# Kernel optimization log

Hardware: AMD Instinct MI355X
Metric: run time of the kernel (lower is better)

Reference implementation:

```python
import jax, jax.numpy as jnp
import numpy as np

NUM_GROUPS = 32
EPS = 1e-6


def group_norm(x, gamma, beta):
    # x: [b, c, h, w]
    b, c, h, w = x.shape
    xg = x.reshape(b, NUM_GROUPS, c // NUM_GROUPS, h, w)
    mean = jnp.mean(xg, axis=(2, 3, 4), keepdims=True)
    var = jnp.var(xg, axis=(2, 3, 4), keepdims=True)
    xn = ((xg - mean) * jax.lax.rsqrt(var + EPS)).reshape(b, c, h, w)
    return xn * gamma[None, :, None, None] + beta[None, :, None, None]


def setup_inputs() -> dict:
    key = jax.random.key(0)
    ks = jax.random.split(key, 8)
    B, C, H, W = 4, 512, 64, 64
    s = 0.02  # small init so softmax is well-conditioned
    return {
        "x": jax.random.normal(ks[0], (B, C, H, W), dtype=jnp.float32),
        "gamma": jnp.ones((C,), dtype=jnp.float32),
        "beta": jnp.zeros((C,), dtype=jnp.float32),
        "wq": jax.random.normal(ks[1], (C, C), dtype=jnp.float32) * s,
        "bq": jnp.zeros((C,), dtype=jnp.float32),
        "wk": jax.random.normal(ks[2], (C, C), dtype=jnp.float32) * s,
        "bk": jnp.zeros((C,), dtype=jnp.float32),
        "wv": jax.random.normal(ks[3], (C, C), dtype=jnp.float32) * s,
        "bv": jnp.zeros((C,), dtype=jnp.float32),
        "wp": jax.random.normal(ks[4], (C, C), dtype=jnp.float32) * s,
        "bp": jnp.zeros((C,), dtype=jnp.float32),
    }


def reference(x, gamma, beta, wq, bq, wk, bk, wv, bv, wp, bp):
    b, c, h, w = x.shape
    hw = h * w
    h_ = group_norm(x, gamma, beta).reshape(b, c, hw)  # [b, c, hw]
    # 1x1 convs == channel matmuls
    q = jnp.einsum('oc,bcn->bon', wq, h_) + bq[None, :, None]
    k = jnp.einsum('oc,bcn->bon', wk, h_) + bk[None, :, None]
    v = jnp.einsum('oc,bcn->bon', wv, h_) + bv[None, :, None]
    # scores[b, n, m] = sum_c q[b,c,n] k[b,c,m]
    scores = jnp.einsum('bcn,bcm->bnm', q, k) * (c ** -0.5)
    attn = jax.nn.softmax(scores, axis=2)  # over keys m
    # out[b, c, n] = sum_m v[b,c,m] * attn[b,n,m]
    o = jnp.einsum('bcm,bnm->bcn', v, attn)
    o = jnp.einsum('oc,bcn->bon', wp, o) + bp[None, :, None]
    return x + o.reshape(b, c, h, w)
```

## Files before the change

kernel.cpp:

```cpp
#include <hip/hip_runtime.h>
#include <hip/hip_bf16.h>

constexpr int BATCH = 4;
constexpr int CH    = 512;
constexpr int HWN   = 4096;
constexpr int NG    = 32;
constexpr float SM_SCALE = 0.044194173824159216f;
constexpr float SM_L2E   = 0.06376608440f;

__device__ __align__(256) ushort g_ht[(long)BATCH*HWN*CH];
__device__ __align__(256) ushort g_qt[(long)BATCH*HWN*CH];
__device__ __align__(256) ushort g_kt[(long)BATCH*HWN*CH];
__device__ __align__(256) ushort g_v [(long)BATCH*CH*HWN];
__device__ __align__(256) ushort g_S [(long)BATCH*HWN*HWN];
__device__ __align__(256) ushort g_ot[(long)BATCH*HWN*CH];
__device__ __align__(256) ushort g_wq[CH*CH], g_wk[CH*CH], g_wv[CH*CH], g_wp[CH*CH];
__device__ float g_mean[BATCH*NG], g_rstd[BATCH*NG];
__device__ float g_rowsum[BATCH*HWN];

typedef short v8s __attribute__((ext_vector_type(8)));
typedef float f32x4 __attribute__((ext_vector_type(4)));

__device__ inline ushort f2b(float f){
  __hip_bfloat16 h = __float2bfloat16(f);
  return __builtin_bit_cast(ushort, h);
}

__device__ inline void gload16(const ushort* g, ushort* lds_base){
  __builtin_amdgcn_global_load_lds(
      (const __attribute__((address_space(1))) unsigned int*)g,
      (__attribute__((address_space(3))) unsigned int*)lds_base, 16, 0, 0);
}

__global__ __launch_bounds__(256) void prep_weights(const float* wq, const float* wk,
                                                    const float* wv, const float* wp){
  int t = blockIdx.x*256 + threadIdx.x;
  g_wq[t] = f2b(wq[t]);
  g_wk[t] = f2b(wk[t]);
  g_wv[t] = f2b(wv[t]);
  g_wp[t] = f2b(wp[t]);
  if (t < BATCH*HWN) g_rowsum[t] = 0.0f;
}

__global__ __launch_bounds__(256) void gn_stats(const float* x){
  __shared__ float ss[4], ss2[4];
  const float4* p = (const float4*)(x + (long)blockIdx.x*65536);
  float s = 0.f, s2 = 0.f;
  for (int i = threadIdx.x; i < 16384; i += 256){
    float4 v = p[i];
    s  += v.x + v.y + v.z + v.w;
    s2 += v.x*v.x + v.y*v.y + v.z*v.z + v.w*v.w;
  }
  for (int off = 1; off < 64; off <<= 1){
    s  += __shfl_xor(s,  off);
    s2 += __shfl_xor(s2, off);
  }
  if ((threadIdx.x & 63) == 0){ ss[threadIdx.x>>6] = s; ss2[threadIdx.x>>6] = s2; }
  __syncthreads();
  if (threadIdx.x == 0){
    float S1 = ss[0]+ss[1]+ss[2]+ss[3], S2 = ss2[0]+ss2[1]+ss2[2]+ss2[3];
    float mean = S1 * (1.0f/65536.0f);
    float var  = S2 * (1.0f/65536.0f) - mean*mean;
    g_mean[blockIdx.x] = mean;
    g_rstd[blockIdx.x] = rsqrtf(var + 1e-6f);
  }
}

__global__ __launch_bounds__(256) void gn_apply(const float* x, const float* gamma, const float* beta){
  __shared__ ushort tile[64][72];
  const int b = blockIdx.z, tc = blockIdx.y, tn = blockIdx.x;
  const int t = threadIdx.x;
  const int r = t >> 4;
  const int ncol = (t & 15) * 4;
  const float* xb = x + ((long)b*CH + tc*64)*HWN + tn*64;
  #pragma unroll
  for (int rg = 0; rg < 4; rg++){
    int c_local = rg*16 + r;
    int c = tc*64 + c_local;
    int gidx = b*NG + (c >> 4);
    float mean = g_mean[gidx], rstd = g_rstd[gidx];
    float ga = gamma[c], be = beta[c];
    float4 v = *(const float4*)(xb + (long)c_local*HWN + ncol);
    tile[c_local][ncol+0] = f2b((v.x - mean)*rstd*ga + be);
    tile[c_local][ncol+1] = f2b((v.y - mean)*rstd*ga + be);
    tile[c_local][ncol+2] = f2b((v.z - mean)*rstd*ga + be);
    tile[c_local][ncol+3] = f2b((v.w - mean)*rstd*ga + be);
  }
  __syncthreads();
  ushort* ht = g_ht + ((long)b*HWN + tn*64)*CH + tc*64;
  #pragma unroll
  for (int rg = 0; rg < 4; rg++){
    int n_local = rg*16 + r;
    int cl = (t & 15) * 4;
    ushort4 pk;
    pk.x = tile[cl+0][n_local];
    pk.y = tile[cl+1][n_local];
    pk.z = tile[cl+2][n_local];
    pk.w = tile[cl+3][n_local];
    *(ushort4*)(ht + (long)n_local*CH + cl) = pk;
  }
}

template<int CFG>
__global__ __launch_bounds__(256, 2) void gemm_bt(const float* bias, const float* xres, float* outf){
  constexpr int Kdim = (CFG==4) ? HWN : CH;
  constexpr int BIAS = (CFG==0 || CFG==1) ? 2 : (CFG==2) ? 1 : 0;

  __shared__ __align__(16) ushort As[128*32];
  __shared__ __align__(16) ushort Bs[128*32];

  const int z = blockIdx.z;
  const int tm = blockIdx.x, tn = blockIdx.y;
  const int t = threadIdx.x;

  const ushort *Ap, *Bp;  ushort* Cp = nullptr;
  int lda, ldb, ldc = 0;
  if constexpr (CFG==0){ Ap=g_ht+(long)z*HWN*CH; Bp=g_wq; Cp=g_qt+(long)z*HWN*CH; lda=CH;  ldb=CH;  ldc=CH;  }
  if constexpr (CFG==1){ Ap=g_ht+(long)z*HWN*CH; Bp=g_wk; Cp=g_kt+(long)z*HWN*CH; lda=CH;  ldb=CH;  ldc=CH;  }
  if constexpr (CFG==2){ Ap=g_wv; Bp=g_ht+(long)z*HWN*CH; Cp=g_v +(long)z*CH*HWN; lda=CH;  ldb=CH;  ldc=HWN; }
  if constexpr (CFG==3){ Ap=g_qt+(long)z*HWN*CH; Bp=g_kt+(long)z*HWN*CH; Cp=g_S+(long)z*HWN*HWN; lda=CH; ldb=CH; ldc=HWN; }
  if constexpr (CFG==4){ Ap=g_S +(long)z*HWN*HWN; Bp=g_v+(long)z*CH*HWN; Cp=g_ot+(long)z*HWN*CH; lda=HWN; ldb=HWN; ldc=CH; }
  if constexpr (CFG==5){ Ap=g_ot+(long)z*HWN*CH; Bp=g_wp; lda=CH; ldb=CH; }

  const int lane = t & 63, wid = t >> 6;
  const int wr = (wid >> 1) * 64, wc = (wid & 1) * 64;
  const int lr = lane & 15, lk = lane >> 4;

  const int srow = t >> 2, sko = t & 3;
  const int wave_base = (t & 192) * 8;

  f32x4 acc[4][4] = {};

  for (int kt = 0; kt < Kdim; kt += 32){
    __syncthreads();
    #pragma unroll
    for (int i = 0; i < 2; i++){
      int row = srow + i*64;
      const ushort* ga = Ap + (long)(tm*128 + row)*lda + kt + sko*8;
      const ushort* gb = Bp + (long)(tn*128 + row)*ldb + kt + sko*8;
      gload16(ga, As + wave_base + i*256*8);
      gload16(gb, Bs + wave_base + i*256*8);
    }
    __syncthreads();
    v8s af[4], bfr[4];
    #pragma unroll
    for (int mi = 0; mi < 4; mi++){
      int row = wr + mi*16 + lr;
      af[mi] = *(const v8s*)(As + row*32 + lk*8);
    }
    #pragma unroll
    for (int ni = 0; ni < 4; ni++){
      int row = wc + ni*16 + lr;
      bfr[ni] = *(const v8s*)(Bs + row*32 + lk*8);
    }
    #pragma unroll
    for (int mi = 0; mi < 4; mi++)
      #pragma unroll
      for (int ni = 0; ni < 4; ni++)
        acc[mi][ni] = __builtin_amdgcn_mfma_f32_16x16x32_bf16(af[mi], bfr[ni], acc[mi][ni], 0, 0, 0);
  }

  if constexpr (CFG==3){
    float rs[4][4] = {};
    #pragma unroll
    for (int mi = 0; mi < 4; mi++){
      #pragma unroll
      for (int ni = 0; ni < 4; ni++){
        int col = tn*128 + wc + ni*16 + lr;
        #pragma unroll
        for (int j = 0; j < 4; j++){
          float p = exp2f(acc[mi][ni][j] * SM_L2E);
          int rowm = tm*128 + wr + mi*16 + lk*4 + j;
          Cp[(long)rowm*ldc + col] = f2b(p);
          rs[mi][j] += p;
        }
      }
    }
    #pragma unroll
    for (int mi = 0; mi < 4; mi++)
      #pragma unroll
      for (int j = 0; j < 4; j++){
        float s = rs[mi][j];
        s += __shfl_xor(s, 1); s += __shfl_xor(s, 2);
        s += __shfl_xor(s, 4); s += __shfl_xor(s, 8);
        rs[mi][j] = s;
      }
    if (lr == 0){
      float* rsum = g_rowsum + (long)z*HWN;
      #pragma unroll
      for (int mi = 0; mi < 4; mi++)
        #pragma unroll
        for (int j = 0; j < 4; j++)
          atomicAdd(&rsum[tm*128 + wr + mi*16 + lk*4 + j], rs[mi][j]);
    }
  } else if constexpr (CFG==5){
    float* ob = outf + (long)z*CH*HWN;
    const float* xb = xres + (long)z*CH*HWN;
    #pragma unroll
    for (int mi = 0; mi < 4; mi++){
      #pragma unroll
      for (int ni = 0; ni < 4; ni++){
        int col = tn*128 + wc + ni*16 + lr;
        int rowm = tm*128 + wr + mi*16 + lk*4;
        float cb = bias[col];
        long off = (long)col*HWN + rowm;
        float4 xv = *(const float4*)(xb + off);
        float4 ov;
        ov.x = acc[mi][ni][0] + cb + xv.x;
        ov.y = acc[mi][ni][1] + cb + xv.y;
        ov.z = acc[mi][ni][2] + cb + xv.z;
        ov.w = acc[mi][ni][3] + cb + xv.w;
        *(float4*)(ob + off) = ov;
      }
    }
  } else {
    const float* rsum = (CFG==4) ? (g_rowsum + (long)z*HWN) : nullptr;
    #pragma unroll
    for (int mi = 0; mi < 4; mi++){
      float inv[4];
      if constexpr (CFG==4){
        int rowb = tm*128 + wr + mi*16 + lk*4;
        float4 s4 = *(const float4*)(rsum + rowb);
        inv[0] = 1.0f/s4.x; inv[1] = 1.0f/s4.y; inv[2] = 1.0f/s4.z; inv[3] = 1.0f/s4.w;
      }
      #pragma unroll
      for (int ni = 0; ni < 4; ni++){
        int col = tn*128 + wc + ni*16 + lr;
        float cb = 0.f;
        if constexpr (BIAS==2) cb = bias[col];
        #pragma unroll
        for (int j = 0; j < 4; j++){
          int rowm = tm*128 + wr + mi*16 + lk*4 + j;
          float v = acc[mi][ni][j];
          if constexpr (CFG==4) v *= inv[j];
          if constexpr (BIAS==1) v += bias[rowm]; else v += cb;
          Cp[(long)rowm*ldc + col] = f2b(v);
        }
      }
    }
  }
}

extern "C" void kernel_launch(void* const* d_in, const int* in_sizes, int n_in,
                              void* d_out, int out_size, void* d_ws, size_t ws_size,
                              hipStream_t stream){
  const float* x     = (const float*)d_in[0];
  const float* gamma = (const float*)d_in[1];
  const float* beta  = (const float*)d_in[2];
  const float* wq    = (const float*)d_in[3];
  const float* bq    = (const float*)d_in[4];
  const float* wk    = (const float*)d_in[5];
  const float* bk    = (const float*)d_in[6];
  const float* wv    = (const float*)d_in[7];
  const float* bv    = (const float*)d_in[8];
  const float* wp    = (const float*)d_in[9];
  const float* bp    = (const float*)d_in[10];
  float* out = (float*)d_out;

  prep_weights<<<1024, 256, 0, stream>>>(wq, wk, wv, wp);
  gn_stats<<<BATCH*NG, 256, 0, stream>>>(x);
  gn_apply<<<dim3(HWN/64, CH/64, BATCH), 256, 0, stream>>>(x, gamma, beta);

  gemm_bt<0><<<dim3(HWN/128, CH/128, BATCH), 256, 0, stream>>>(bq, nullptr, nullptr);
  gemm_bt<1><<<dim3(HWN/128, CH/128, BATCH), 256, 0, stream>>>(bk, nullptr, nullptr);
  gemm_bt<2><<<dim3(CH/128, HWN/128, BATCH), 256, 0, stream>>>(bv, nullptr, nullptr);
  gemm_bt<3><<<dim3(HWN/128, HWN/128, BATCH), 256, 0, stream>>>(nullptr, nullptr, nullptr);
  gemm_bt<4><<<dim3(HWN/128, CH/128, BATCH), 256, 0, stream>>>(nullptr, nullptr, nullptr);
  gemm_bt<5><<<dim3(HWN/128, CH/128, BATCH), 256, 0, stream>>>(bp, x, out);
}
```

Measured before the change: 406.2 us.

## Replace attention score and PV GEMMs with 256-tile pipelined LDS-swizzled kernel

Adds a new 512-thread GEMM kernel with 256-row tiles, double-buffered direct-to-LDS loads, XOR-swizzled LDS layout, and fine-grained barrier/vmcnt scheduling that interleaves staging with MFMA work. It is used for the QK^T (with exp and rowsum epilogue) and the S·V (with normalization) GEMMs, which dominate runtime. The aim is better data reuse per tile, fewer LDS bank conflicts, and overlapping global loads with compute. It raises register and LDS pressure and relies on hand-tuned waitcnt counts for correctness.

```diff
diff --git a/kernel.cpp b/kernel.cpp
--- a/kernel.cpp
+++ b/kernel.cpp
@@ -30,6 +30,12 @@
   __builtin_amdgcn_global_load_lds(
       (const __attribute__((address_space(1))) unsigned int*)g,
       (__attribute__((address_space(3))) unsigned int*)lds_base, 16, 0, 0);
+}
+
+__device__ inline void blockbar(){
+  asm volatile("" ::: "memory");
+  __builtin_amdgcn_s_barrier();
+  asm volatile("" ::: "memory");
 }
 
 __global__ __launch_bounds__(256) void prep_weights(const float* wq, const float* wk,
@@ -103,7 +109,7 @@
 
 template<int CFG>
 __global__ __launch_bounds__(256, 2) void gemm_bt(const float* bias, const float* xres, float* outf){
-  constexpr int Kdim = (CFG==4) ? HWN : CH;
+  constexpr int Kdim = CH;
   constexpr int BIAS = (CFG==0 || CFG==1) ? 2 : (CFG==2) ? 1 : 0;
 
   __shared__ __align__(16) ushort As[128*32];
@@ -118,8 +124,6 @@
   if constexpr (CFG==0){ Ap=g_ht+(long)z*HWN*CH; Bp=g_wq; Cp=g_qt+(long)z*HWN*CH; lda=CH;  ldb=CH;  ldc=CH;  }
   if constexpr (CFG==1){ Ap=g_ht+(long)z*HWN*CH; Bp=g_wk; Cp=g_kt+(long)z*HWN*CH; lda=CH;  ldb=CH;  ldc=CH;  }
   if constexpr (CFG==2){ Ap=g_wv; Bp=g_ht+(long)z*HWN*CH; Cp=g_v +(long)z*CH*HWN; lda=CH;  ldb=CH;  ldc=HWN; }
-  if constexpr (CFG==3){ Ap=g_qt+(long)z*HWN*CH; Bp=g_kt+(long)z*HWN*CH; Cp=g_S+(long)z*HWN*HWN; lda=CH; ldb=CH; ldc=HWN; }
-  if constexpr (CFG==4){ Ap=g_S +(long)z*HWN*HWN; Bp=g_v+(long)z*CH*HWN; Cp=g_ot+(long)z*HWN*CH; lda=HWN; ldb=HWN; ldc=CH; }
   if constexpr (CFG==5){ Ap=g_ot+(long)z*HWN*CH; Bp=g_wp; lda=CH; ldb=CH; }
 
   const int lane = t & 63, wid = t >> 6;
@@ -160,40 +164,7 @@
         acc[mi][ni] = __builtin_amdgcn_mfma_f32_16x16x32_bf16(af[mi], bfr[ni], acc[mi][ni], 0, 0, 0);
   }
 
-  if constexpr (CFG==3){
-    float rs[4][4] = {};
-    #pragma unroll
-    for (int mi = 0; mi < 4; mi++){
-      #pragma unroll
-      for (int ni = 0; ni < 4; ni++){
-        int col = tn*128 + wc + ni*16 + lr;
-        #pragma unroll
-        for (int j = 0; j < 4; j++){
-          float p = exp2f(acc[mi][ni][j] * SM_L2E);
-          int rowm = tm*128 + wr + mi*16 + lk*4 + j;
-          Cp[(long)rowm*ldc + col] = f2b(p);
-          rs[mi][j] += p;
-        }
-      }
-    }
-    #pragma unroll
-    for (int mi = 0; mi < 4; mi++)
-      #pragma unroll
-      for (int j = 0; j < 4; j++){
-        float s = rs[mi][j];
-        s += __shfl_xor(s, 1); s += __shfl_xor(s, 2);
-        s += __shfl_xor(s, 4); s += __shfl_xor(s, 8);
-        rs[mi][j] = s;
-      }
-    if (lr == 0){
-      float* rsum = g_rowsum + (long)z*HWN;
-      #pragma unroll
-      for (int mi = 0; mi < 4; mi++)
-        #pragma unroll
-        for (int j = 0; j < 4; j++)
-          atomicAdd(&rsum[tm*128 + wr + mi*16 + lk*4 + j], rs[mi][j]);
-    }
-  } else if constexpr (CFG==5){
+  if constexpr (CFG==5){
     float* ob = outf + (long)z*CH*HWN;
     const float* xb = xres + (long)z*CH*HWN;
     #pragma unroll
@@ -214,15 +185,8 @@
       }
     }
   } else {
-    const float* rsum = (CFG==4) ? (g_rowsum + (long)z*HWN) : nullptr;
     #pragma unroll
     for (int mi = 0; mi < 4; mi++){
-      float inv[4];
-      if constexpr (CFG==4){
-        int rowb = tm*128 + wr + mi*16 + lk*4;
-        float4 s4 = *(const float4*)(rsum + rowb);
-        inv[0] = 1.0f/s4.x; inv[1] = 1.0f/s4.y; inv[2] = 1.0f/s4.z; inv[3] = 1.0f/s4.w;
-      }
       #pragma unroll
       for (int ni = 0; ni < 4; ni++){
         int col = tn*128 + wc + ni*16 + lr;
@@ -232,10 +196,199 @@
         for (int j = 0; j < 4; j++){
           int rowm = tm*128 + wr + mi*16 + lk*4 + j;
           float v = acc[mi][ni][j];
-          if constexpr (CFG==4) v *= inv[j];
           if constexpr (BIAS==1) v += bias[rowm]; else v += cb;
           Cp[(long)rowm*ldc + col] = f2b(v);
         }
+      }
+    }
+  }
+}
+
+template<int CFG>
+__global__ __launch_bounds__(512, 2) void gemm256(){
+  constexpr int Kdim = (CFG==4) ? HWN : CH;
+  constexpr int BN   = (CFG==3) ? 256 : 128;
+  constexpr int NI   = BN/64;
+  constexpr int NI2  = NI/2;
+  constexpr int AUNITS = 2048;
+  constexpr int BUNITS = BN*64/8;
+  constexpr int BH   = BUNITS/2;
+  constexpr int BBIT = (CFG==3) ? 5 : 4;
+  constexpr int Lb   = BH/512;
+  constexpr int DBUF = AUNITS + BUNITS;
+  constexpr int NT = Kdim/64, NITER = NT/2;
+
+  __shared__ __align__(16) ushort lds[DBUF*2*8];
+
+  const int t = threadIdx.x, lane = t & 63, wid = t >> 6;
+  const int wm = wid >> 2, wn = wid & 3;
+  const int lr = lane & 15, lk = lane >> 4;
+  const int tm = blockIdx.x, tn = blockIdx.y, z = blockIdx.z;
+
+  const ushort *Ap, *Bp; ushort* Cp; long lda, ldb, ldc;
+  if constexpr (CFG==3){
+    Ap = g_qt + (long)z*HWN*CH; lda = CH;
+    Bp = g_kt + (long)z*HWN*CH; ldb = CH;
+    Cp = g_S  + (long)z*HWN*HWN; ldc = HWN;
+  } else {
+    Ap = g_S  + (long)z*HWN*HWN; lda = HWN;
+    Bp = g_v  + (long)z*CH*HWN;  ldb = HWN;
+    Cp = g_ot + (long)z*HWN*CH;  ldc = CH;
+  }
+
+  const int srw  = lane >> 3;
+  const int sc16 = (lane & 7) ^ srw;
+  const int rxor = lr & 7;
+
+  auto stageA = [&](int h, int T){
+    #pragma unroll
+    for (int j = 0; j < 2; j++){
+      int W = wid*2 + j;
+      int RH = W*8 + srw;
+      int r = (RH>>6)*128 + h*64 + (RH&63);
+      gload16(Ap + (long)(tm*256 + r)*lda + T*64 + sc16*8,
+              lds + ((T&1)*DBUF + h*1024 + W*64)*8);
+    }
+  };
+  auto stageB = [&](int h, int T){
+    #pragma unroll
+    for (int j = 0; j < Lb; j++){
+      int W = wid*Lb + j;
+      int RH = W*8 + srw;
+      int r = (RH>>BBIT)*(2<<BBIT) + h*(1<<BBIT) + (RH & ((1<<BBIT)-1));
+      gload16(Bp + (long)(tn*BN + r)*ldb + T*64 + sc16*8,
+              lds + ((T&1)*DBUF + AUNITS + h*BH + W*64)*8);
+    }
+  };
+  auto readA = [&](int d, int h, v8s (&a)[4][2]){
+    #pragma unroll
+    for (int mp = 0; mp < 4; mp++){
+      int RH = wm*64 + mp*16 + lr;
+      #pragma unroll
+      for (int kk = 0; kk < 2; kk++){
+        int u = d*DBUF + h*1024 + RH*8 + ((kk*4 + lk) ^ rxor);
+        a[mp][kk] = *(const v8s*)(lds + u*8);
+      }
+    }
+  };
+  auto readB = [&](int d, int h, v8s (&b)[NI2][2]){
+    #pragma unroll
+    for (int np = 0; np < NI2; np++){
+      int RH = (CFG==3) ? (wn*32 + np*16 + lr) : (wn*16 + lr);
+      #pragma unroll
+      for (int kk = 0; kk < 2; kk++){
+        int u = d*DBUF + AUNITS + h*BH + RH*8 + ((kk*4 + lk) ^ rxor);
+        b[np][kk] = *(const v8s*)(lds + u*8);
+      }
+    }
+  };
+
+  f32x4 acc[8][NI] = {};
+  auto mm = [&](const v8s (&a)[4][2], const v8s (&b)[NI2][2], int mh, int nh){
+    __builtin_amdgcn_s_setprio(1);
+    #pragma unroll
+    for (int mp = 0; mp < 4; mp++)
+      #pragma unroll
+      for (int np = 0; np < NI2; np++)
+        #pragma unroll
+        for (int kk = 0; kk < 2; kk++)
+          acc[mh*4+mp][nh*NI2+np] = __builtin_amdgcn_mfma_f32_16x16x32_bf16(
+              a[mp][kk], b[np][kk], acc[mh*4+mp][nh*NI2+np], 0, 0, 0);
+    __builtin_amdgcn_s_setprio(0);
+  };
+
+  #define VM_STEADY() do { if constexpr (CFG==3) asm volatile("s_waitcnt vmcnt(4)" ::: "memory"); \
+                           else                  asm volatile("s_waitcnt vmcnt(3)" ::: "memory"); } while(0)
+  #define VM_DRAIN()  asm volatile("s_waitcnt vmcnt(0)" ::: "memory")
+
+  stageA(0, 0); stageB(0, 0); stageA(1, 0); stageB(1, 0); stageA(0, 1); stageB(0, 1);
+  VM_STEADY();
+  blockbar();
+
+  for (int it = 0; it < NITER; ++it){
+    const int X = 2*it, Y = X + 1;
+    const bool last = (it == NITER-1);
+    v8s a[4][2], b[NI2][2];
+
+    stageA(1, Y);
+    readA(0, 0, a); readB(0, 0, b);
+    mm(a, b, 0, 0);
+    blockbar();
+    stageB(1, Y);
+    readA(0, 1, a);
+    mm(a, b, 1, 0);
+    blockbar();
+    if (!last) stageB(0, X+2);
+    readB(0, 1, b); readA(0, 0, a);
+    mm(a, b, 0, 1);
+    blockbar();
+    if (!last) stageA(0, X+2);
+    readA(0, 1, a);
+    mm(a, b, 1, 1);
+    if (last) VM_DRAIN(); else VM_STEADY();
+    blockbar();
+    if (!last) stageA(1, X+2);
+    readA(1, 0, a); readB(1, 0, b);
+    mm(a, b, 0, 0);
+    blockbar();
+    if (!last) stageB(1, X+2);
+    readA(1, 1, a);
+    mm(a, b, 1, 0);
+    blockbar();
+    if (!last) stageB(0, Y+2);
+    readB(1, 1, b); readA(1, 0, a);
+    mm(a, b, 0, 1);
+    blockbar();
+    if (!last) stageA(0, Y+2);
+    readA(1, 1, a);
+    mm(a, b, 1, 1);
+    if (!last) VM_STEADY();
+    blockbar();
+  }
+  #undef VM_STEADY
+  #undef VM_DRAIN
+
+  if constexpr (CFG==3){
+    float rs[8][4] = {};
+    #pragma unroll
+    for (int mi = 0; mi < 8; mi++){
+      #pragma unroll
+      for (int ni = 0; ni < NI; ni++){
+        int col = tn*256 + wn*64 + ni*16 + lr;
+        #pragma unroll
+        for (int j = 0; j < 4; j++){
+          float p = exp2f(acc[mi][ni][j] * SM_L2E);
+          int row = tm*256 + wm*128 + mi*16 + lk*4 + j;
+          Cp[(long)row*ldc + col] = f2b(p);
+          rs[mi][j] += p;
+        }
+      }
+    }
+    float* rsum = g_rowsum + (long)z*HWN;
+    #pragma unroll
+    for (int mi = 0; mi < 8; mi++){
+      #pragma unroll
+      for (int j = 0; j < 4; j++){
+        float s = rs[mi][j];
+        s += __shfl_xor(s, 1); s += __shfl_xor(s, 2);
+        s += __shfl_xor(s, 4); s += __shfl_xor(s, 8);
+        if (lr == 0)
+          atomicAdd(&rsum[tm*256 + wm*128 + mi*16 + lk*4 + j], s);
+      }
+    }
+  } else {
+    const float* rsum = g_rowsum + (long)z*HWN;
+    #pragma unroll
+    for (int mi = 0; mi < 8; mi++){
+      int rowb = tm*256 + wm*128 + mi*16 + lk*4;
+      float4 s4 = *(const float4*)(rsum + rowb);
+      float inv[4] = {1.0f/s4.x, 1.0f/s4.y, 1.0f/s4.z, 1.0f/s4.w};
+      #pragma unroll
+      for (int ni = 0; ni < NI; ni++){
+        int col = tn*BN + wn*32 + ni*16 + lr;
+        #pragma unroll
+        for (int j = 0; j < 4; j++)
+          Cp[(long)(rowb + j)*ldc + col] = f2b(acc[mi][ni][j] * inv[j]);
       }
     }
   }
@@ -264,7 +417,7 @@
   gemm_bt<0><<<dim3(HWN/128, CH/128, BATCH), 256, 0, stream>>>(bq, nullptr, nullptr);
   gemm_bt<1><<<dim3(HWN/128, CH/128, BATCH), 256, 0, stream>>>(bk, nullptr, nullptr);
   gemm_bt<2><<<dim3(CH/128, HWN/128, BATCH), 256, 0, stream>>>(bv, nullptr, nullptr);
-  gemm_bt<3><<<dim3(HWN/128, HWN/128, BATCH), 256, 0, stream>>>(nullptr, nullptr, nullptr);
-  gemm_bt<4><<<dim3(HWN/128, CH/128, BATCH), 256, 0, stream>>>(nullptr, nullptr, nullptr);
+  gemm256<3><<<dim3(HWN/256, HWN/256, BATCH), 512, 0, stream>>>();
+  gemm256<4><<<dim3(HWN/256, CH/128, BATCH), 512, 0, stream>>>();
   gemm_bt<5><<<dim3(HWN/128, CH/128, BATCH), 256, 0, stream>>>(bp, x, out);
 }
```

After: 419.7 us. 1.03x slower.

## Fuse QK^T, softmax and PV into a flash-style attention kernel; merge Q/K projections

Applied to the files above, without the earlier changes.

Replaces the separate scores GEMM (which wrote a full bf16 HWN x HWN matrix plus atomically accumulated row sums) and the PV GEMM with a single fused attention kernel. It streams K and V tiles through double-buffered LDS via direct global-to-LDS loads, computes exp scores in registers, stages P in swizzled LDS and accumulates P·V. Q and K projections are merged into one GEMM against a concatenated weight. This removes the large HBM round trip of the score matrix. Like the old code it applies no max subtraction, and each block keeps 16 Q fragments in registers, which may limit occupancy.

```diff
diff --git a/kernel.cpp b/kernel.cpp
--- a/kernel.cpp
+++ b/kernel.cpp
@@ -9,14 +9,13 @@
 constexpr float SM_L2E   = 0.06376608440f;
 
 __device__ __align__(256) ushort g_ht[(long)BATCH*HWN*CH];
-__device__ __align__(256) ushort g_qt[(long)BATCH*HWN*CH];
-__device__ __align__(256) ushort g_kt[(long)BATCH*HWN*CH];
+__device__ __align__(256) ushort g_qk[(long)BATCH*HWN*1024];
 __device__ __align__(256) ushort g_v [(long)BATCH*CH*HWN];
-__device__ __align__(256) ushort g_S [(long)BATCH*HWN*HWN];
 __device__ __align__(256) ushort g_ot[(long)BATCH*HWN*CH];
-__device__ __align__(256) ushort g_wq[CH*CH], g_wk[CH*CH], g_wv[CH*CH], g_wp[CH*CH];
+__device__ __align__(256) ushort g_wqk[2*CH*CH];
+__device__ __align__(256) ushort g_wv[CH*CH], g_wp[CH*CH];
+__device__ float g_bqk[2*CH];
 __device__ float g_mean[BATCH*NG], g_rstd[BATCH*NG];
-__device__ float g_rowsum[BATCH*HWN];
 
 typedef short v8s __attribute__((ext_vector_type(8)));
 typedef float f32x4 __attribute__((ext_vector_type(4)));
@@ -33,13 +32,14 @@
 }
 
 __global__ __launch_bounds__(256) void prep_weights(const float* wq, const float* wk,
-                                                    const float* wv, const float* wp){
+                                                    const float* wv, const float* wp,
+                                                    const float* bq, const float* bk){
   int t = blockIdx.x*256 + threadIdx.x;
-  g_wq[t] = f2b(wq[t]);
-  g_wk[t] = f2b(wk[t]);
+  g_wqk[t]        = f2b(wq[t]);
+  g_wqk[CH*CH+t]  = f2b(wk[t]);
   g_wv[t] = f2b(wv[t]);
   g_wp[t] = f2b(wp[t]);
-  if (t < BATCH*HWN) g_rowsum[t] = 0.0f;
+  if (t < 2*CH) g_bqk[t] = (t < CH) ? bq[t] : bk[t-CH];
 }
 
 __global__ __launch_bounds__(256) void gn_stats(const float* x){
@@ -103,8 +103,7 @@
 
 template<int CFG>
 __global__ __launch_bounds__(256, 2) void gemm_bt(const float* bias, const float* xres, float* outf){
-  constexpr int Kdim = (CFG==4) ? HWN : CH;
-  constexpr int BIAS = (CFG==0 || CFG==1) ? 2 : (CFG==2) ? 1 : 0;
+  constexpr int Kdim = CH;
 
   __shared__ __align__(16) ushort As[128*32];
   __shared__ __align__(16) ushort Bs[128*32];
@@ -114,12 +113,9 @@
   const int t = threadIdx.x;
 
   const ushort *Ap, *Bp;  ushort* Cp = nullptr;
-  int lda, ldb, ldc = 0;
-  if constexpr (CFG==0){ Ap=g_ht+(long)z*HWN*CH; Bp=g_wq; Cp=g_qt+(long)z*HWN*CH; lda=CH;  ldb=CH;  ldc=CH;  }
-  if constexpr (CFG==1){ Ap=g_ht+(long)z*HWN*CH; Bp=g_wk; Cp=g_kt+(long)z*HWN*CH; lda=CH;  ldb=CH;  ldc=CH;  }
-  if constexpr (CFG==2){ Ap=g_wv; Bp=g_ht+(long)z*HWN*CH; Cp=g_v +(long)z*CH*HWN; lda=CH;  ldb=CH;  ldc=HWN; }
-  if constexpr (CFG==3){ Ap=g_qt+(long)z*HWN*CH; Bp=g_kt+(long)z*HWN*CH; Cp=g_S+(long)z*HWN*HWN; lda=CH; ldb=CH; ldc=HWN; }
-  if constexpr (CFG==4){ Ap=g_S +(long)z*HWN*HWN; Bp=g_v+(long)z*CH*HWN; Cp=g_ot+(long)z*HWN*CH; lda=HWN; ldb=HWN; ldc=CH; }
+  long lda, ldb, ldc = 0;
+  if constexpr (CFG==0){ Ap=g_ht+(long)z*HWN*CH; Bp=g_wqk; Cp=g_qk+(long)z*HWN*1024; lda=CH; ldb=CH; ldc=1024; }
+  if constexpr (CFG==2){ Ap=g_wv; Bp=g_ht+(long)z*HWN*CH; Cp=g_v +(long)z*CH*HWN; lda=CH; ldb=CH; ldc=HWN; }
   if constexpr (CFG==5){ Ap=g_ot+(long)z*HWN*CH; Bp=g_wp; lda=CH; ldb=CH; }
 
   const int lane = t & 63, wid = t >> 6;
@@ -160,40 +156,7 @@
         acc[mi][ni] = __builtin_amdgcn_mfma_f32_16x16x32_bf16(af[mi], bfr[ni], acc[mi][ni], 0, 0, 0);
   }
 
-  if constexpr (CFG==3){
-    float rs[4][4] = {};
-    #pragma unroll
-    for (int mi = 0; mi < 4; mi++){
-      #pragma unroll
-      for (int ni = 0; ni < 4; ni++){
-        int col = tn*128 + wc + ni*16 + lr;
-        #pragma unroll
-        for (int j = 0; j < 4; j++){
-          float p = exp2f(acc[mi][ni][j] * SM_L2E);
-          int rowm = tm*128 + wr + mi*16 + lk*4 + j;
-          Cp[(long)rowm*ldc + col] = f2b(p);
-          rs[mi][j] += p;
-        }
-      }
-    }
-    #pragma unroll
-    for (int mi = 0; mi < 4; mi++)
-      #pragma unroll
-      for (int j = 0; j < 4; j++){
-        float s = rs[mi][j];
-        s += __shfl_xor(s, 1); s += __shfl_xor(s, 2);
-        s += __shfl_xor(s, 4); s += __shfl_xor(s, 8);
-        rs[mi][j] = s;
-      }
-    if (lr == 0){
-      float* rsum = g_rowsum + (long)z*HWN;
-      #pragma unroll
-      for (int mi = 0; mi < 4; mi++)
-        #pragma unroll
-        for (int j = 0; j < 4; j++)
-          atomicAdd(&rsum[tm*128 + wr + mi*16 + lk*4 + j], rs[mi][j]);
-    }
-  } else if constexpr (CFG==5){
+  if constexpr (CFG==5){
     float* ob = outf + (long)z*CH*HWN;
     const float* xb = xres + (long)z*CH*HWN;
     #pragma unroll
@@ -214,28 +177,152 @@
       }
     }
   } else {
-    const float* rsum = (CFG==4) ? (g_rowsum + (long)z*HWN) : nullptr;
     #pragma unroll
     for (int mi = 0; mi < 4; mi++){
-      float inv[4];
-      if constexpr (CFG==4){
-        int rowb = tm*128 + wr + mi*16 + lk*4;
-        float4 s4 = *(const float4*)(rsum + rowb);
-        inv[0] = 1.0f/s4.x; inv[1] = 1.0f/s4.y; inv[2] = 1.0f/s4.z; inv[3] = 1.0f/s4.w;
-      }
       #pragma unroll
       for (int ni = 0; ni < 4; ni++){
         int col = tn*128 + wc + ni*16 + lr;
         float cb = 0.f;
-        if constexpr (BIAS==2) cb = bias[col];
+        if constexpr (CFG==0) cb = g_bqk[col];
         #pragma unroll
         for (int j = 0; j < 4; j++){
           int rowm = tm*128 + wr + mi*16 + lk*4 + j;
           float v = acc[mi][ni][j];
-          if constexpr (CFG==4) v *= inv[j];
-          if constexpr (BIAS==1) v += bias[rowm]; else v += cb;
+          if constexpr (CFG==2) v += bias[rowm]; else v += cb;
           Cp[(long)rowm*ldc + col] = f2b(v);
         }
+      }
+    }
+  }
+}
+
+__global__ __launch_bounds__(512, 2) void fused_attn(){
+  constexpr int NITER = HWN/32;
+  __shared__ __align__(16) ushort Kl[2][32*512];
+  __shared__ __align__(16) ushort Vl[2][512*32];
+  __shared__ __align__(16) ushort Pl[64*32];
+  __shared__ float rs_lds[2][64];
+
+  const int t = threadIdx.x, lane = t & 63, wid = t >> 6;
+  const int lr = lane & 15, lk = lane >> 4;
+  const int qn = wid >> 1, qm2 = wid & 1;
+  const int ntile = blockIdx.x, z = blockIdx.y;
+  const ushort* qk = g_qk + (long)z*HWN*1024;
+  const ushort* vv = g_v  + (long)z*CH*HWN;
+
+  v8s q[16];
+  {
+    const ushort* qrow = qk + (long)(ntile*64 + qn*16 + lr)*1024 + lk*8;
+    #pragma unroll
+    for (int s = 0; s < 16; s++) q[s] = *(const v8s*)(qrow + s*32);
+  }
+
+  auto stageK = [&](int kvt){
+    ushort* dst = &Kl[kvt & 1][0] + wid*64*8;
+    #pragma unroll
+    for (int j = 0; j < 4; j++){
+      int u = j*512 + t;
+      int m = u >> 6, slot = u & 63;
+      gload16(qk + 512 + (long)(kvt*32 + m)*1024 + 8*(slot ^ (m & 7)), dst + j*512*8);
+    }
+  };
+  auto stageV = [&](int kvt){
+    ushort* dst = &Vl[kvt & 1][0] + wid*64*8;
+    #pragma unroll
+    for (int j = 0; j < 4; j++){
+      int u = j*512 + t;
+      int c = u >> 2, slot = u & 3;
+      gload16(vv + (long)c*HWN + kvt*32 + 8*(slot ^ (c & 3)), dst + j*512*8);
+    }
+  };
+
+  stageK(0); stageV(0);
+  asm volatile("s_waitcnt vmcnt(0)" ::: "memory");
+  __builtin_amdgcn_s_barrier();
+
+  f32x4 acc[4][4] = {};
+  float rs4[4] = {0.f, 0.f, 0.f, 0.f};
+
+  for (int kvt = 0; kvt < NITER; kvt++){
+    if (kvt + 1 < NITER){ stageK(kvt+1); stageV(kvt+1); }
+    const ushort* Kb = &Kl[kvt & 1][0];
+    const ushort* Vb = &Vl[kvt & 1][0];
+
+    f32x4 sc[4] = {};
+    {
+      const int mrow = qm2*16 + lr;
+      __builtin_amdgcn_s_setprio(1);
+      #pragma unroll
+      for (int s = 0; s < 16; s++){
+        v8s kf = *(const v8s*)(Kb + (mrow*64 + ((s*4 + lk) ^ (lr & 7)))*8);
+        sc[s & 3] = __builtin_amdgcn_mfma_f32_16x16x32_bf16(q[s], kf, sc[s & 3], 0, 0, 0);
+      }
+      __builtin_amdgcn_s_setprio(0);
+    }
+    f32x4 sv = sc[0] + sc[1] + sc[2] + sc[3];
+
+    #pragma unroll
+    for (int j = 0; j < 4; j++){
+      float p = exp2f(sv[j] * SM_L2E);
+      int n = qn*16 + lk*4 + j;
+      int m = qm2*16 + lr;
+      *(ushort*)((char*)Pl + n*64 + ((((m >> 3) ^ (n & 3)) << 4) | ((m & 7) * 2))) = f2b(p);
+      rs4[j] += p;
+    }
+
+    asm volatile("s_waitcnt lgkmcnt(0)" ::: "memory");
+    __builtin_amdgcn_s_barrier();
+
+    {
+      v8s pa[4], vb[4];
+      #pragma unroll
+      for (int fn = 0; fn < 4; fn++){
+        int n = fn*16 + lr;
+        pa[fn] = *(const v8s*)((char*)Pl + n*64 + ((lk ^ (n & 3)) << 4));
+      }
+      #pragma unroll
+      for (int fc = 0; fc < 4; fc++){
+        int c = wid*64 + fc*16 + lr;
+        vb[fc] = *(const v8s*)(Vb + (c*4 + (lk ^ (c & 3)))*8);
+      }
+      __builtin_amdgcn_s_setprio(1);
+      #pragma unroll
+      for (int fn = 0; fn < 4; fn++)
+        #pragma unroll
+        for (int fc = 0; fc < 4; fc++)
+          acc[fn][fc] = __builtin_amdgcn_mfma_f32_16x16x32_bf16(pa[fn], vb[fc], acc[fn][fc], 0, 0, 0);
+      __builtin_amdgcn_s_setprio(0);
+    }
+
+    asm volatile("s_waitcnt vmcnt(0)" ::: "memory");
+    __builtin_amdgcn_s_barrier();
+  }
+
+  #pragma unroll
+  for (int j = 0; j < 4; j++){
+    float s = rs4[j];
+    s += __shfl_xor(s, 1); s += __shfl_xor(s, 2);
+    s += __shfl_xor(s, 4); s += __shfl_xor(s, 8);
+    rs4[j] = s;
+  }
+  if (lr == 0){
+    #pragma unroll
+    for (int j = 0; j < 4; j++)
+      rs_lds[qm2][qn*16 + lk*4 + j] = rs4[j];
+  }
+  __syncthreads();
+
+  ushort* ot = g_ot + ((long)z*HWN + ntile*64)*CH;
+  #pragma unroll
+  for (int fn = 0; fn < 4; fn++){
+    #pragma unroll
+    for (int j = 0; j < 4; j++){
+      int n = fn*16 + lk*4 + j;
+      float inv = 1.0f / (rs_lds[0][n] + rs_lds[1][n]);
+      #pragma unroll
+      for (int fc = 0; fc < 4; fc++){
+        int c = wid*64 + fc*16 + lr;
+        ot[(long)n*CH + c] = f2b(acc[fn][fc][j] * inv);
       }
     }
   }
@@ -257,14 +344,12 @@
   const float* bp    = (const float*)d_in[10];
   float* out = (float*)d_out;
 
-  prep_weights<<<1024, 256, 0, stream>>>(wq, wk, wv, wp);
+  prep_weights<<<1024, 256, 0, stream>>>(wq, wk, wv, wp, bq, bk);
   gn_stats<<<BATCH*NG, 256, 0, stream>>>(x);
   gn_apply<<<dim3(HWN/64, CH/64, BATCH), 256, 0, stream>>>(x, gamma, beta);
 
-  gemm_bt<0><<<dim3(HWN/128, CH/128, BATCH), 256, 0, stream>>>(bq, nullptr, nullptr);
-  gemm_bt<1><<<dim3(HWN/128, CH/128, BATCH), 256, 0, stream>>>(bk, nullptr, nullptr);
+  gemm_bt<0><<<dim3(HWN/128, 1024/128, BATCH), 256, 0, stream>>>(nullptr, nullptr, nullptr);
   gemm_bt<2><<<dim3(CH/128, HWN/128, BATCH), 256, 0, stream>>>(bv, nullptr, nullptr);
-  gemm_bt<3><<<dim3(HWN/128, HWN/128, BATCH), 256, 0, stream>>>(nullptr, nullptr, nullptr);
-  gemm_bt<4><<<dim3(HWN/128, CH/128, BATCH), 256, 0, stream>>>(nullptr, nullptr, nullptr);
+  fused_attn<<<dim3(HWN/64, BATCH), 512, 0, stream>>>();
   gemm_bt<5><<<dim3(HWN/128, CH/128, BATCH), 256, 0, stream>>>(bp, x, out);
 }
```

New measurement: 451.6 us. 1.11x slower.
